# Optimization experiments

Measured on AMD Instinct MI355X. Metric: run time of the kernel, lower is better.

The kernel has to match this reference:

```python
import jax, jax.numpy as jnp
import numpy as np

NUM_STATES = 3
MAX_ITERS = 20
EPS = 1e-8
STATE_PRIOR = jnp.array([0.1, 0.8, 0.1], dtype=jnp.float32)
TRANS = jnp.array([[0.98, 0.01, 0.01],
                   [0.01, 0.98, 0.01],
                   [0.01, 0.01, 0.98]], dtype=jnp.float32)

N_SPOTS = 20000
N_GENES = 3000
N_EDGES = 120000


def setup_inputs() -> dict:
    key = jax.random.key(0)
    k1, k2, k3 = jax.random.split(key, 3)
    norm_x = jax.random.uniform(k1, (N_SPOTS, N_GENES), dtype=jnp.float32)
    reconstructed_features = jax.random.uniform(k2, (N_SPOTS, N_GENES), dtype=jnp.float32)
    edge_index = jax.random.randint(k3, (2, N_EDGES), 0, N_SPOTS, dtype=jnp.int32)
    return {"norm_x": norm_x, "reconstructed_features": reconstructed_features,
            "edge_index": edge_index}


def _mcmc_state_probs(spot_mean, m, key):
    """Vectorized Metropolis-Hastings over all samples.

    spot_mean: (N,) standardized per-spot mean (detached)
    m:         (N,) raw per-spot feature means (detached)
    Faithful quirk of the original: likelihood(state, mean) indexes mean[state]
    where state in {0,1,2}, i.e. it uses the means of the FIRST num_states
    SAMPLES as the per-state gaussian centers, and sums over all spots.
    """
    # L[s] = sum_j exp(-0.5 * (spot_mean_j - m[s])^2), s = 0..NUM_STATES-1
    L = jnp.sum(jnp.exp(-0.5 * (spot_mean[None, :] - m[:NUM_STATES, None]) ** 2), axis=1)  # (3,)
    N = spot_mean.shape[0]
    k0, kloop = jax.random.split(key)
    states0 = jax.random.randint(k0, (N,), 0, NUM_STATES)

    def step(states, k):
        k1, k2 = jax.random.split(k)
        cand = jax.random.randint(k1, (N,), 0, NUM_STATES)
        prior_ratio = STATE_PRIOR[cand] / STATE_PRIOR[states]
        lik_ratio = L[cand] / L[states]
        trans_ratio = TRANS[states, cand] / TRANS[cand, states]
        acc = prior_ratio * lik_ratio * trans_ratio
        u = jax.random.uniform(k2, (N,))
        new_states = jnp.where(u < acc, cand, states)
        return new_states, jax.nn.one_hot(new_states, NUM_STATES, dtype=jnp.float32)

    keys = jax.random.split(kloop, MAX_ITERS)
    _, onehots = jax.lax.scan(step, states0, keys)  # (MAX_ITERS, N, 3)
    return jnp.sum(onehots, axis=0)  # (N, 3) visit counts = state_probs


def reference(norm_x, reconstructed_features, edge_index):
    N = reconstructed_features.shape[0]
    # per-spot mean, detached (original does .detach().cpu().numpy())
    m = jax.lax.stop_gradient(jnp.mean(reconstructed_features, axis=1))  # (N,)
    spot_mean = (m - m.mean()) / (m.std() + EPS)

    state_probs = _mcmc_state_probs(spot_mean, m, jax.random.key(42))  # (N, 3)

    # scatter_mean(state_probs[row], col) over the spatial graph
    row, col = edge_index[0], edge_index[1]
    sums = jax.ops.segment_sum(state_probs[row], col, num_segments=N)          # (N, 3)
    cnt = jax.ops.segment_sum(jnp.ones(row.shape, jnp.float32), col, num_segments=N)
    smoothed = sums / jnp.maximum(cnt, 1.0)[:, None]

    final_states = jnp.argmax(smoothed, axis=1).astype(jnp.float32) + 1.0      # (N,)

    adj = reconstructed_features * final_states[:, None]                       # (N, G)
    copy_sum = jnp.sum(adj, axis=1, keepdims=True)
    pseudo_sum = jnp.sum(norm_x, axis=1, keepdims=True)
    norm_copy = adj / (copy_sum + EPS) * pseudo_sum

    # range endpoints are detached (.item() in torch); inner min/max are not
    rmin = jax.lax.stop_gradient(norm_copy.min()) * 0.8
    rmax = jax.lax.stop_gradient(norm_copy.max()) * 1.2
    norm_copy = (norm_copy - norm_copy.min()) / (norm_copy.max() - norm_copy.min() + EPS)
    norm_copy = norm_copy * (rmax - rmin) + rmin
    norm_copy = norm_copy / jnp.mean(norm_copy)

    reg_loss = jnp.sum(reconstructed_features ** 2) * 1e-4
    return norm_copy, reg_loss
```

## Files before the change

kernel.cpp:

```cpp
#include <hip/hip_runtime.h>
#include <cmath>


static constexpr int NS = 20000;
static constexpr int NG = 3000;
static constexpr int G4 = NG / 4;
static constexpr float EPS = 1e-8f;

typedef float fv4 __attribute__((ext_vector_type(4)));


__global__ __launch_bounds__(256) void k_p(const fv4* __restrict__ nx,
                                           float* __restrict__ P)
{
    const int row  = blockIdx.x * 4 + (threadIdx.x >> 6);
    const int lane = threadIdx.x & 63;
    const fv4* n = nx + (size_t)row * G4;
    float p = 0.f;
    for (int c = lane; c < G4; c += 64) {
        fv4 b = __builtin_nontemporal_load(n + c);
        p += (b.x + b.y) + (b.z + b.w);
    }
    #pragma unroll
    for (int off = 32; off > 0; off >>= 1) p += __shfl_down(p, off);
    if (lane == 0) P[row] = p;
}

__global__ __launch_bounds__(256) void k_rfstats(const fv4* __restrict__ rf,
                                                 float* __restrict__ S,
                                                 float* __restrict__ MN,
                                                 float* __restrict__ MX,
                                                 float* __restrict__ Q)
{
    const int row  = blockIdx.x * 4 + (threadIdx.x >> 6);
    const int lane = threadIdx.x & 63;
    const fv4* r = rf + (size_t)row * G4;
    float s = 0.f, q = 0.f, mn = INFINITY, mx = -INFINITY;
    for (int c = lane; c < G4; c += 64) {
        fv4 a = r[c];
        s += (a.x + a.y) + (a.z + a.w);
        q += a.x * a.x + a.y * a.y + a.z * a.z + a.w * a.w;
        mn = fminf(mn, fminf(fminf(a.x, a.y), fminf(a.z, a.w)));
        mx = fmaxf(mx, fmaxf(fmaxf(a.x, a.y), fmaxf(a.z, a.w)));
    }
    #pragma unroll
    for (int off = 32; off > 0; off >>= 1) {
        s += __shfl_down(s, off);
        q += __shfl_down(q, off);
        mn = fminf(mn, __shfl_down(mn, off));
        mx = fmaxf(mx, __shfl_down(mx, off));
    }
    if (lane == 0) { S[row] = s; Q[row] = q; MN[row] = mn; MX[row] = mx; }
}

__global__ __launch_bounds__(256) void k_scalars(
    const fv4* __restrict__ S4, const fv4* __restrict__ P4,
    const fv4* __restrict__ MN4, const fv4* __restrict__ MX4,
    const fv4* __restrict__ Q4,
    float* __restrict__ AB, float* __restrict__ loss_out)
{
    double st = 0.0, sq = 0.0;
    float tmn = INFINITY, tmx = -INFINITY;
    for (int i = threadIdx.x; i < NS / 4; i += 256) {
        fv4 s = S4[i], p = P4[i], mn = MN4[i], mx = MX4[i], q = Q4[i];
        float sc0 = p.x / (s.x + EPS), sc1 = p.y / (s.y + EPS);
        float sc2 = p.z / (s.z + EPS), sc3 = p.w / (s.w + EPS);
        st += (double)(sc0 * s.x) + (double)(sc1 * s.y)
            + (double)(sc2 * s.z) + (double)(sc3 * s.w);
        sq += (double)q.x + (double)q.y + (double)q.z + (double)q.w;
        tmn = fminf(tmn, fminf(fminf(mn.x * sc0, mn.y * sc1), fminf(mn.z * sc2, mn.w * sc3)));
        tmx = fmaxf(tmx, fmaxf(fmaxf(mx.x * sc0, mx.y * sc1), fmaxf(mx.z * sc2, mx.w * sc3)));
    }
    #pragma unroll
    for (int off = 32; off > 0; off >>= 1) {
        st += __shfl_down(st, off);
        sq += __shfl_down(sq, off);
        tmn = fminf(tmn, __shfl_down(tmn, off));
        tmx = fmaxf(tmx, __shfl_down(tmx, off));
    }
    __shared__ double lst[4], lsq[4];
    __shared__ float lmn[4], lmx[4];
    const int wid = threadIdx.x >> 6;
    if ((threadIdx.x & 63) == 0) { lst[wid] = st; lsq[wid] = sq; lmn[wid] = tmn; lmx[wid] = tmx; }
    __syncthreads();
    if (threadIdx.x == 0) {
        st  = (lst[0] + lst[1]) + (lst[2] + lst[3]);
        sq  = (lsq[0] + lsq[1]) + (lsq[2] + lsq[3]);
        tmn = fminf(fminf(lmn[0], lmn[1]), fminf(lmn[2], lmn[3]));
        tmx = fmaxf(fmaxf(lmx[0], lmx[1]), fmaxf(lmx[2], lmx[3]));
        const float rmin = tmn * 0.8f;
        const float rmax = tmx * 1.2f;
        const float a = (rmax - rmin) / (tmx - tmn + EPS);
        const float mean_t = (float)(st / (double)((long long)NS * (long long)NG));
        const float mean_u = (mean_t - tmn) * a + rmin;
        AB[0] = a / mean_u;
        AB[1] = (rmin - tmn * a) / mean_u;
        *loss_out = (float)(sq * 1e-4);
    }
}

__global__ __launch_bounds__(256) void k_finalize(
    const fv4* __restrict__ rf,
    const float* __restrict__ S, const float* __restrict__ P,
    const float* __restrict__ AB,
    fv4* __restrict__ out)
{
    const int row = blockIdx.x;
    const float A = AB[0], B = AB[1];
    const float c = (P[row] / (S[row] + EPS)) * A;
    const fv4* r = rf + (size_t)row * G4;
    fv4* o = out + (size_t)row * G4;
    for (int i = threadIdx.x; i < G4; i += 256) {
        fv4 a = r[i];
        fv4 v;
        v.x = fmaf(a.x, c, B);
        v.y = fmaf(a.y, c, B);
        v.z = fmaf(a.z, c, B);
        v.w = fmaf(a.w, c, B);
        __builtin_nontemporal_store(v, o + i);
    }
}

extern "C" void kernel_launch(void* const* d_in, const int* in_sizes, int n_in,
                              void* d_out, int out_size, void* d_ws, size_t ws_size,
                              hipStream_t stream) {
    const float* nx = (const float*)d_in[0];
    const float* rf = (const float*)d_in[1];
    float* out = (float*)d_out;
    float* ws = (float*)d_ws;
    float* S  = ws;
    float* P  = ws + NS;
    float* MN = ws + 2 * NS;
    float* MX = ws + 3 * NS;
    float* Q  = ws + 4 * NS;
    float* AB = ws + 5 * NS;
    float* loss_out = out + (out_size - 1);

    k_p      <<<NS / 4, 256, 0, stream>>>((const fv4*)nx, P);
    k_rfstats<<<NS / 4, 256, 0, stream>>>((const fv4*)rf, S, MN, MX, Q);
    k_scalars<<<1, 256, 0, stream>>>((const fv4*)S, (const fv4*)P,
                                     (const fv4*)MN, (const fv4*)MX,
                                     (const fv4*)Q, AB, loss_out);
    k_finalize<<<NS, 256, 0, stream>>>((const fv4*)rf, S, P, AB, (fv4*)out);
}
```

Measured before the change: 161.1 us.

## Fuse per-row stats kernels and pre-reduce global scalars per block

Merges the two per-row reduction kernels into one that reads norm_x and reconstructed_features in the same pass. Each warp now handles four rows, and each block writes partial sum, sum of squares, min and max, so the single-block scalar kernel reduces 1250 partials instead of 20000 rows. The finalize kernel switches to one wave per row with four rows per block. The aim is to cut launch overhead and serial work in the single-block kernel, at the cost of lower grid parallelism in the stats kernel and float instead of double accumulation within blocks.

Result: faster. 151.0 us, median of 2 (-6.3%).

```diff
diff --git a/kernel.cpp b/kernel.cpp
--- a/kernel.cpp
+++ b/kernel.cpp
@@ -5,71 +5,78 @@
 static constexpr int NS = 20000;
 static constexpr int NG = 3000;
 static constexpr int G4 = NG / 4;
+static constexpr int NW = NS / 4;
+static constexpr int NB = NW / 4;
 static constexpr float EPS = 1e-8f;
 
 typedef float fv4 __attribute__((ext_vector_type(4)));
 
 
-__global__ __launch_bounds__(256) void k_p(const fv4* __restrict__ nx,
-                                           float* __restrict__ P)
+__global__ __launch_bounds__(256) void k_stats(
+    const fv4* __restrict__ nx, const fv4* __restrict__ rf,
+    float* __restrict__ S, float* __restrict__ P,
+    float* __restrict__ PST, float* __restrict__ PSQ,
+    float* __restrict__ PMN, float* __restrict__ PMX)
 {
-    const int row  = blockIdx.x * 4 + (threadIdx.x >> 6);
+    const int wid  = threadIdx.x >> 6;
     const int lane = threadIdx.x & 63;
-    const fv4* n = nx + (size_t)row * G4;
-    float p = 0.f;
-    for (int c = lane; c < G4; c += 64) {
-        fv4 b = __builtin_nontemporal_load(n + c);
-        p += (b.x + b.y) + (b.z + b.w);
+    const int gw   = blockIdx.x * 4 + wid;
+    float st = 0.f, sq = 0.f, tmn = INFINITY, tmx = -INFINITY;
+    #pragma unroll
+    for (int k = 0; k < 4; ++k) {
+        const int row = gw + k * NW;
+        const fv4* r = rf + (size_t)row * G4;
+        const fv4* n = nx + (size_t)row * G4;
+        float s = 0.f, p = 0.f, q = 0.f, mn = INFINITY, mx = -INFINITY;
+        for (int c = lane; c < G4; c += 64) {
+            fv4 a = r[c];
+            fv4 b = __builtin_nontemporal_load(n + c);
+            s += (a.x + a.y) + (a.z + a.w);
+            q += a.x * a.x + a.y * a.y + a.z * a.z + a.w * a.w;
+            mn = fminf(mn, fminf(fminf(a.x, a.y), fminf(a.z, a.w)));
+            mx = fmaxf(mx, fmaxf(fmaxf(a.x, a.y), fmaxf(a.z, a.w)));
+            p += (b.x + b.y) + (b.z + b.w);
+        }
+        #pragma unroll
+        for (int off = 32; off > 0; off >>= 1) {
+            s += __shfl_down(s, off);
+            p += __shfl_down(p, off);
+            q += __shfl_down(q, off);
+            mn = fminf(mn, __shfl_down(mn, off));
+            mx = fmaxf(mx, __shfl_down(mx, off));
+        }
+        if (lane == 0) {
+            S[row] = s; P[row] = p;
+            const float sc = p / (s + EPS);
+            st += sc * s;
+            sq += q;
+            tmn = fminf(tmn, mn * sc);
+            tmx = fmaxf(tmx, mx * sc);
+        }
     }
-    #pragma unroll
-    for (int off = 32; off > 0; off >>= 1) p += __shfl_down(p, off);
-    if (lane == 0) P[row] = p;
-}
-
-__global__ __launch_bounds__(256) void k_rfstats(const fv4* __restrict__ rf,
-                                                 float* __restrict__ S,
-                                                 float* __restrict__ MN,
-                                                 float* __restrict__ MX,
-                                                 float* __restrict__ Q)
-{
-    const int row  = blockIdx.x * 4 + (threadIdx.x >> 6);
-    const int lane = threadIdx.x & 63;
-    const fv4* r = rf + (size_t)row * G4;
-    float s = 0.f, q = 0.f, mn = INFINITY, mx = -INFINITY;
-    for (int c = lane; c < G4; c += 64) {
-        fv4 a = r[c];
-        s += (a.x + a.y) + (a.z + a.w);
-        q += a.x * a.x + a.y * a.y + a.z * a.z + a.w * a.w;
-        mn = fminf(mn, fminf(fminf(a.x, a.y), fminf(a.z, a.w)));
-        mx = fmaxf(mx, fmaxf(fmaxf(a.x, a.y), fmaxf(a.z, a.w)));
+    __shared__ float lst[4], lsq[4], lmn[4], lmx[4];
+    if (lane == 0) { lst[wid] = st; lsq[wid] = sq; lmn[wid] = tmn; lmx[wid] = tmx; }
+    __syncthreads();
+    if (threadIdx.x == 0) {
+        PST[blockIdx.x] = (lst[0] + lst[1]) + (lst[2] + lst[3]);
+        PSQ[blockIdx.x] = (lsq[0] + lsq[1]) + (lsq[2] + lsq[3]);
+        PMN[blockIdx.x] = fminf(fminf(lmn[0], lmn[1]), fminf(lmn[2], lmn[3]));
+        PMX[blockIdx.x] = fmaxf(fmaxf(lmx[0], lmx[1]), fmaxf(lmx[2], lmx[3]));
     }
-    #pragma unroll
-    for (int off = 32; off > 0; off >>= 1) {
-        s += __shfl_down(s, off);
-        q += __shfl_down(q, off);
-        mn = fminf(mn, __shfl_down(mn, off));
-        mx = fmaxf(mx, __shfl_down(mx, off));
-    }
-    if (lane == 0) { S[row] = s; Q[row] = q; MN[row] = mn; MX[row] = mx; }
 }
 
 __global__ __launch_bounds__(256) void k_scalars(
-    const fv4* __restrict__ S4, const fv4* __restrict__ P4,
-    const fv4* __restrict__ MN4, const fv4* __restrict__ MX4,
-    const fv4* __restrict__ Q4,
+    const float* __restrict__ PST, const float* __restrict__ PSQ,
+    const float* __restrict__ PMN, const float* __restrict__ PMX,
     float* __restrict__ AB, float* __restrict__ loss_out)
 {
     double st = 0.0, sq = 0.0;
     float tmn = INFINITY, tmx = -INFINITY;
-    for (int i = threadIdx.x; i < NS / 4; i += 256) {
-        fv4 s = S4[i], p = P4[i], mn = MN4[i], mx = MX4[i], q = Q4[i];
-        float sc0 = p.x / (s.x + EPS), sc1 = p.y / (s.y + EPS);
-        float sc2 = p.z / (s.z + EPS), sc3 = p.w / (s.w + EPS);
-        st += (double)(sc0 * s.x) + (double)(sc1 * s.y)
-            + (double)(sc2 * s.z) + (double)(sc3 * s.w);
-        sq += (double)q.x + (double)q.y + (double)q.z + (double)q.w;
-        tmn = fminf(tmn, fminf(fminf(mn.x * sc0, mn.y * sc1), fminf(mn.z * sc2, mn.w * sc3)));
-        tmx = fmaxf(tmx, fmaxf(fmaxf(mx.x * sc0, mx.y * sc1), fmaxf(mx.z * sc2, mx.w * sc3)));
+    for (int i = threadIdx.x; i < NB; i += 256) {
+        st += (double)PST[i];
+        sq += (double)PSQ[i];
+        tmn = fminf(tmn, PMN[i]);
+        tmx = fmaxf(tmx, PMX[i]);
     }
     #pragma unroll
     for (int off = 32; off > 0; off >>= 1) {
@@ -105,12 +112,13 @@
     const float* __restrict__ AB,
     fv4* __restrict__ out)
 {
-    const int row = blockIdx.x;
+    const int row  = blockIdx.x * 4 + (threadIdx.x >> 6);
+    const int lane = threadIdx.x & 63;
     const float A = AB[0], B = AB[1];
     const float c = (P[row] / (S[row] + EPS)) * A;
     const fv4* r = rf + (size_t)row * G4;
     fv4* o = out + (size_t)row * G4;
-    for (int i = threadIdx.x; i < G4; i += 256) {
+    for (int i = lane; i < G4; i += 64) {
         fv4 a = r[i];
         fv4 v;
         v.x = fmaf(a.x, c, B);
@@ -127,19 +135,18 @@
     const float* nx = (const float*)d_in[0];
     const float* rf = (const float*)d_in[1];
     float* out = (float*)d_out;
-    float* ws = (float*)d_ws;
-    float* S  = ws;
-    float* P  = ws + NS;
-    float* MN = ws + 2 * NS;
-    float* MX = ws + 3 * NS;
-    float* Q  = ws + 4 * NS;
-    float* AB = ws + 5 * NS;
+    float* ws  = (float*)d_ws;
+    float* S   = ws;
+    float* P   = ws + NS;
+    float* PST = ws + 2 * NS;
+    float* PSQ = PST + NB;
+    float* PMN = PST + 2 * NB;
+    float* PMX = PST + 3 * NB;
+    float* AB  = PST + 4 * NB;
     float* loss_out = out + (out_size - 1);
 
-    k_p      <<<NS / 4, 256, 0, stream>>>((const fv4*)nx, P);
-    k_rfstats<<<NS / 4, 256, 0, stream>>>((const fv4*)rf, S, MN, MX, Q);
-    k_scalars<<<1, 256, 0, stream>>>((const fv4*)S, (const fv4*)P,
-                                     (const fv4*)MN, (const fv4*)MX,
-                                     (const fv4*)Q, AB, loss_out);
-    k_finalize<<<NS, 256, 0, stream>>>((const fv4*)rf, S, P, AB, (fv4*)out);
+    k_stats   <<<NB,     256, 0, stream>>>((const fv4*)nx, (const fv4*)rf,
+                                           S, P, PST, PSQ, PMN, PMX);
+    k_scalars <<<1,      256, 0, stream>>>(PST, PSQ, PMN, PMX, AB, loss_out);
+    k_finalize<<<NS / 4, 256, 0, stream>>>((const fv4*)rf, S, P, AB, (fv4*)out);
 }
```
